# Optimization experiments

Measured on AMD Instinct MI355X. Metric: run time of the kernel, lower is better.

## Reference

```python
import jax, jax.numpy as jnp
import numpy as np

B = 256      # batch
C = 512      # num_classes (independent heads)
F = 768      # BERT pooler_output dim (hard-coded in module)
D = 512      # dense_layer_size


def setup_inputs() -> dict:
    key = jax.random.key(0)
    ks = jax.random.split(key, 7)
    s1 = 1.0 / np.sqrt(F)
    s2 = 1.0 / np.sqrt(D)
    return {
        "x":  jax.random.normal(ks[0], (B, F), dtype=jnp.float32),
        "W1": jax.random.normal(ks[1], (C, F, D), dtype=jnp.float32) * s1,
        "b1": jax.random.normal(ks[2], (C, D), dtype=jnp.float32) * s1,
        "W2": jax.random.normal(ks[3], (C, D, D), dtype=jnp.float32) * s2,
        "b2": jax.random.normal(ks[4], (C, D), dtype=jnp.float32) * s2,
        "W3": jax.random.normal(ks[5], (C, D, 2), dtype=jnp.float32) * s2,
        "b3": jax.random.normal(ks[6], (C, 2), dtype=jnp.float32) * s2,
    }


def reference(x, W1, b1, W2, b2, W3, b3):
    # Batched version of the per-class Python loop:
    # each head: Linear(F,D)-ReLU-(Dropout=identity in eval)-Linear(D,D)-ReLU-Linear(D,2)
    h = jax.nn.relu(jnp.einsum('bf,cfd->bcd', x, W1) + b1[None])        # [B, C, D]
    h = jax.nn.relu(jnp.einsum('bcd,cde->bce', h, W2) + b2[None])        # [B, C, D]
    out = jnp.einsum('bcd,cde->bce', h, W3) + b3[None]                   # [B, C, 2]
    return out
```

## Files before the change

### kernel.cpp

```cpp
#include <hip/hip_runtime.h>
#include <stdint.h>

typedef float f32x4 __attribute__((ext_vector_type(4)));
typedef float f32x2 __attribute__((ext_vector_type(2)));
typedef short bf16x8 __attribute__((ext_vector_type(8)));
typedef uint32_t u32x4 __attribute__((ext_vector_type(4)));

__device__ __forceinline__ uint32_t bf16_rne(float f) {
  uint32_t x = __float_as_uint(f);
  return (x + 0x7FFFu + ((x >> 16) & 1u)) >> 16;
}

__device__ __forceinline__ void ldsbar() {
  asm volatile("s_waitcnt lgkmcnt(0)\n\ts_barrier" ::: "memory");
}

__global__ void cast_x_kernel(const float* __restrict__ x,
                              uint32_t* __restrict__ xb, int n2) {
  int i = blockIdx.x * 256 + threadIdx.x;
  if (i >= n2) return;
  f32x2 v = *(const f32x2*)(x + 2 * i);
  xb[i] = bf16_rne(v[0]) | (bf16_rne(v[1]) << 16);
}

template <int K, int MODE>
__global__ __launch_bounds__(512, 4) void gemm_fused(
    const uint16_t* __restrict__ Abase, long long aClassStride,
    const float* __restrict__ Wbase, const float* __restrict__ biasBase,
    uint16_t* __restrict__ Hout, const float* __restrict__ W3base,
    float* __restrict__ part) {
  constexpr int NT = K / 64;
  __shared__ uint8_t smem[16384];

  const int tid = threadIdx.x;
  const int bid = blockIdx.x;
  const int logical = ((bid & 7) << 9) | (bid >> 3);
  const int c = logical >> 3;
  const int nt = logical & 7;
  const int n0 = nt * 64;

  const uint16_t* Ab = Abase + (size_t)c * (size_t)aClassStride;
  const float* Wc = Wbase + (size_t)c * (K * 512) + n0;

  const int l = tid & 63, w = tid >> 6;
  const int lr = l & 15, lg = l >> 4;

  const uint16_t* Ap = Ab + (size_t)(w * 32 + lr) * K + lg * 8;

  f32x4 acc[2][4];
#pragma unroll
  for (int i = 0; i < 2; i++)
#pragma unroll
    for (int j = 0; j < 4; j++) acc[i][j] = {0.f, 0.f, 0.f, 0.f};

  auto loadB = [&](int ts, float* g) {
    const float* Ws = Wc + (size_t)(ts * 64 + w * 8) * 512 + l;
#pragma unroll
    for (int r = 0; r < 8; r++) g[r] = Ws[(size_t)r * 512];
  };
  auto loadA = [&](int ts, bf16x8* as) {
#pragma unroll
    for (int kk = 0; kk < 2; ++kk)
#pragma unroll
      for (int mf = 0; mf < 2; mf++)
        as[kk * 2 + mf] =
            *(const bf16x8*)(Ap + ts * 64 + kk * 32 + (size_t)mf * 16 * K);
  };
  auto writeB = [&](const float* g, int buf) {
    u32x4 p;
#pragma unroll
    for (int j = 0; j < 4; j++)
      p[j] = bf16_rne(g[2 * j]) | (bf16_rne(g[2 * j + 1]) << 16);
    *(u32x4*)(smem + buf * 8192 + l * 128 + ((w ^ (l & 7)) << 4)) = p;
  };
  auto comp = [&](int buf, const bf16x8* as) {
    const uint8_t* s = smem + buf * 8192;
#pragma unroll
    for (int kk = 0; kk < 2; ++kk) {
      const int kx = ((lg * 16) ^ ((lr & 7) << 4)) ^ (kk << 6);
      bf16x8 b[4];
#pragma unroll
      for (int nf = 0; nf < 4; nf++)
        b[nf] = *(const bf16x8*)(s + (nf * 16 + lr) * 128 + kx);
#pragma unroll
      for (int mf = 0; mf < 2; mf++)
#pragma unroll
        for (int nf = 0; nf < 4; nf++)
          acc[mf][nf] = __builtin_amdgcn_mfma_f32_16x16x32_bf16(
              as[kk * 2 + mf], b[nf], acc[mf][nf], 0, 0, 0);
    }
  };

  float g[3][8];
  bf16x8 a[2][4];
  loadB(0, g[0]);
  loadB(1, g[1]);
  loadA(0, a[0]);
  writeB(g[0], 0);
  loadA(1, a[1]);
  loadB(2, g[2]);
  ldsbar();

#pragma unroll
  for (int t = 0; t < NT; ++t) {
    comp(t & 1, a[t & 1]);
    if (t + 1 < NT) writeB(g[(t + 1) % 3], (t + 1) & 1);
    if (t + 2 < NT) loadA(t + 2, a[t & 1]);
    if (t + 3 < NT) loadB(t + 3, g[t % 3]);
    if (t + 1 < NT) ldsbar();
  }

  float bv[4];
#pragma unroll
  for (int nf = 0; nf < 4; nf++)
    bv[nf] = biasBase[c * 512 + n0 + nf * 16 + lr];

  if constexpr (MODE == 0) {
    uint16_t* Oc = Hout + (size_t)c * 131072 + n0;
#pragma unroll
    for (int mf = 0; mf < 2; mf++)
#pragma unroll
      for (int nf = 0; nf < 4; nf++)
#pragma unroll
        for (int r = 0; r < 4; r++) {
          int m = w * 32 + mf * 16 + lg * 4 + r;
          float v = fmaxf(acc[mf][nf][r] + bv[nf], 0.f);
          Oc[(size_t)m * 512 + nf * 16 + lr] = (uint16_t)bf16_rne(v);
        }
  } else {
    float w30[4], w31[4];
#pragma unroll
    for (int nf = 0; nf < 4; nf++) {
      f32x2 t = *(const f32x2*)(W3base +
                                ((size_t)c * 512 + n0 + nf * 16 + lr) * 2);
      w30[nf] = t[0];
      w31[nf] = t[1];
    }
#pragma unroll
    for (int mf = 0; mf < 2; mf++)
#pragma unroll
      for (int r = 0; r < 4; r++) {
        float s0 = 0.f, s1 = 0.f;
#pragma unroll
        for (int nf = 0; nf < 4; nf++) {
          float v = fmaxf(acc[mf][nf][r] + bv[nf], 0.f);
          s0 += v * w30[nf];
          s1 += v * w31[nf];
        }
#pragma unroll
        for (int d = 1; d < 16; d <<= 1) {
          s0 += __shfl_xor(s0, d);
          s1 += __shfl_xor(s1, d);
        }
        if (lr == 0) {
          int m = w * 32 + mf * 16 + lg * 4 + r;
          *(f32x2*)(part + (((size_t)c * 256 + m) * 8 + nt) * 2) =
              f32x2{s0, s1};
        }
      }
  }
}

__global__ __launch_bounds__(512) void reduce_out(
    const float* __restrict__ part, const float* __restrict__ b3,
    float* __restrict__ out) {
  const int b = blockIdx.x, c = threadIdx.x;
  const f32x4* p = (const f32x4*)(part + ((size_t)c * 256 + b) * 16);
  f32x4 v0 = p[0], v1 = p[1], v2 = p[2], v3 = p[3];
  float s0 = b3[c * 2] + v0[0] + v0[2] + v1[0] + v1[2] + v2[0] + v2[2] +
             v3[0] + v3[2];
  float s1 = b3[c * 2 + 1] + v0[1] + v0[3] + v1[1] + v1[3] + v2[1] + v2[3] +
             v3[1] + v3[3];
  *(f32x2*)(out + ((size_t)b * 512 + c) * 2) = f32x2{s0, s1};
}

extern "C" void kernel_launch(void* const* d_in, const int* in_sizes, int n_in,
                              void* d_out, int out_size, void* d_ws,
                              size_t ws_size, hipStream_t stream) {
  const float* x = (const float*)d_in[0];
  const float* W1 = (const float*)d_in[1];
  const float* b1 = (const float*)d_in[2];
  const float* W2 = (const float*)d_in[3];
  const float* b2 = (const float*)d_in[4];
  const float* W3 = (const float*)d_in[5];
  const float* b3 = (const float*)d_in[6];
  float* out = (float*)d_out;

  uint8_t* ws = (uint8_t*)d_ws;
  const size_t xb_off = 0;
  const size_t h1_off = 393216;
  const size_t part_off = h1_off + 134217728;
  const size_t need = part_off + 8388608;
  if (ws_size < need) return;

  uint32_t* xb = (uint32_t*)(ws + xb_off);
  uint16_t* h1 = (uint16_t*)(ws + h1_off);
  float* part = (float*)(ws + part_off);

  cast_x_kernel<<<dim3(384), dim3(256), 0, stream>>>(x, xb, 98304);
  gemm_fused<768, 0><<<dim3(4096), dim3(512), 0, stream>>>(
      (const uint16_t*)xb, 0LL, W1, b1, h1, nullptr, nullptr);
  gemm_fused<512, 1><<<dim3(4096), dim3(512), 0, stream>>>(
      h1, 131072LL, W2, b2, nullptr, W3, part);
  reduce_out<<<dim3(256), dim3(512), 0, stream>>>(part, b3, out);
}
```

Measured before the change: 464.8 us.

## Store hidden activations in MFMA fragment order via LDS-staged transpose

The first GEMM now stages its bf16 outputs through a swizzled shared-memory tile and writes them out as 16-byte vectors in a fragment-ordered layout. The second GEMM can then read its A operands as contiguous per-lane vectors instead of strided row loads. B conversion uses the packed v_cvt_pk_bf16_f32 instruction instead of manual rounding, and prologue loads are reordered. Shared memory grows to 48KB and launch bounds drop to 2 blocks per SM, which may reduce occupancy.

```diff
diff --git a/kernel.cpp b/kernel.cpp
--- a/kernel.cpp
+++ b/kernel.cpp
@@ -24,13 +24,12 @@
 }
 
 template <int K, int MODE>
-__global__ __launch_bounds__(512, 4) void gemm_fused(
-    const uint16_t* __restrict__ Abase, long long aClassStride,
-    const float* __restrict__ Wbase, const float* __restrict__ biasBase,
-    uint16_t* __restrict__ Hout, const float* __restrict__ W3base,
-    float* __restrict__ part) {
+__global__ __launch_bounds__(512, 2) void gemm_fused(
+    const uint16_t* __restrict__ Abase, const float* __restrict__ Wbase,
+    const float* __restrict__ biasBase, uint16_t* __restrict__ Hout,
+    const float* __restrict__ W3base, float* __restrict__ part) {
   constexpr int NT = K / 64;
-  __shared__ uint8_t smem[16384];
+  __shared__ uint8_t smem[49152];
 
   const int tid = threadIdx.x;
   const int bid = blockIdx.x;
@@ -39,13 +38,15 @@
   const int nt = logical & 7;
   const int n0 = nt * 64;
 
-  const uint16_t* Ab = Abase + (size_t)c * (size_t)aClassStride;
   const float* Wc = Wbase + (size_t)c * (K * 512) + n0;
-
   const int l = tid & 63, w = tid >> 6;
   const int lr = l & 15, lg = l >> 4;
 
-  const uint16_t* Ap = Ab + (size_t)(w * 32 + lr) * K + lg * 8;
+  const uint16_t* Ap;
+  if constexpr (MODE == 0)
+    Ap = Abase + (size_t)(w * 32 + lr) * 768 + lg * 8;
+  else
+    Ap = Abase + (size_t)c * 131072 + w * 1024 + l * 8;
 
   f32x4 acc[2][4];
 #pragma unroll
@@ -54,23 +55,30 @@
     for (int j = 0; j < 4; j++) acc[i][j] = {0.f, 0.f, 0.f, 0.f};
 
   auto loadB = [&](int ts, float* g) {
-    const float* Ws = Wc + (size_t)(ts * 64 + w * 8) * 512 + l;
-#pragma unroll
-    for (int r = 0; r < 8; r++) g[r] = Ws[(size_t)r * 512];
+    const float* p = Wc + (size_t)(ts * 64 + w * 8) * 512 + l;
+#pragma unroll
+    for (int r = 0; r < 8; r++) g[r] = p[(size_t)r * 512];
   };
   auto loadA = [&](int ts, bf16x8* as) {
 #pragma unroll
     for (int kk = 0; kk < 2; ++kk)
 #pragma unroll
-      for (int mf = 0; mf < 2; mf++)
-        as[kk * 2 + mf] =
-            *(const bf16x8*)(Ap + ts * 64 + kk * 32 + (size_t)mf * 16 * K);
+      for (int mf = 0; mf < 2; mf++) {
+        if constexpr (MODE == 0)
+          as[kk * 2 + mf] = *(const bf16x8*)(Ap + ts * 64 + kk * 32 +
+                                             (size_t)mf * 16 * 768);
+        else
+          as[kk * 2 + mf] =
+              *(const bf16x8*)(Ap + ts * 16384 + kk * 8192 + mf * 512);
+      }
   };
   auto writeB = [&](const float* g, int buf) {
-    u32x4 p;
-#pragma unroll
-    for (int j = 0; j < 4; j++)
-      p[j] = bf16_rne(g[2 * j]) | (bf16_rne(g[2 * j + 1]) << 16);
+    uint32_t p0, p1, p2, p3;
+    asm("v_cvt_pk_bf16_f32 %0, %1, %2" : "=v"(p0) : "v"(g[0]), "v"(g[1]));
+    asm("v_cvt_pk_bf16_f32 %0, %1, %2" : "=v"(p1) : "v"(g[2]), "v"(g[3]));
+    asm("v_cvt_pk_bf16_f32 %0, %1, %2" : "=v"(p2) : "v"(g[4]), "v"(g[5]));
+    asm("v_cvt_pk_bf16_f32 %0, %1, %2" : "=v"(p3) : "v"(g[6]), "v"(g[7]));
+    u32x4 p = {p0, p1, p2, p3};
     *(u32x4*)(smem + buf * 8192 + l * 128 + ((w ^ (l & 7)) << 4)) = p;
   };
   auto comp = [&](int buf, const bf16x8* as) {
@@ -96,9 +104,9 @@
   loadB(0, g[0]);
   loadB(1, g[1]);
   loadA(0, a[0]);
+  loadB(2, g[2]);
+  loadA(1, a[1]);
   writeB(g[0], 0);
-  loadA(1, a[1]);
-  loadB(2, g[2]);
   ldsbar();
 
 #pragma unroll
@@ -116,17 +124,28 @@
     bv[nf] = biasBase[c * 512 + n0 + nf * 16 + lr];
 
   if constexpr (MODE == 0) {
-    uint16_t* Oc = Hout + (size_t)c * 131072 + n0;
+    uint8_t* T = smem + 16384 + w * 4096;
 #pragma unroll
     for (int mf = 0; mf < 2; mf++)
 #pragma unroll
       for (int nf = 0; nf < 4; nf++)
 #pragma unroll
         for (int r = 0; r < 4; r++) {
-          int m = w * 32 + mf * 16 + lg * 4 + r;
+          int m = mf * 16 + lg * 4 + r;
           float v = fmaxf(acc[mf][nf][r] + bv[nf], 0.f);
-          Oc[(size_t)m * 512 + nf * 16 + lr] = (uint16_t)bf16_rne(v);
-        }
+          *(uint16_t*)(T + m * 128 + (((nf * 16 + lr) * 2) ^ ((m & 7) << 4))) =
+              (uint16_t)bf16_rne(v);
+        }
+    uint16_t* Hc = Hout + (size_t)c * 131072 + nt * 16384 + w * 1024 + l * 8;
+#pragma unroll
+    for (int kk = 0; kk < 2; kk++)
+#pragma unroll
+      for (int mf = 0; mf < 2; mf++) {
+        int m = mf * 16 + lr;
+        bf16x8 hv = *(const bf16x8*)(T + m * 128 +
+                                     ((kk * 64 + lg * 16) ^ ((m & 7) << 4)));
+        *(bf16x8*)(Hc + kk * 8192 + mf * 512) = hv;
+      }
   } else {
     float w30[4], w31[4];
 #pragma unroll
@@ -194,13 +213,13 @@
   if (ws_size < need) return;
 
   uint32_t* xb = (uint32_t*)(ws + xb_off);
-  uint16_t* h1 = (uint16_t*)(ws + h1_off);
+  uint16_t* h1f = (uint16_t*)(ws + h1_off);
   float* part = (float*)(ws + part_off);
 
   cast_x_kernel<<<dim3(384), dim3(256), 0, stream>>>(x, xb, 98304);
   gemm_fused<768, 0><<<dim3(4096), dim3(512), 0, stream>>>(
-      (const uint16_t*)xb, 0LL, W1, b1, h1, nullptr, nullptr);
+      (const uint16_t*)xb, W1, b1, h1f, nullptr, nullptr);
   gemm_fused<512, 1><<<dim3(4096), dim3(512), 0, stream>>>(
-      h1, 131072LL, W2, b2, nullptr, W3, part);
+      h1f, W2, b2, nullptr, W3, part);
   reduce_out<<<dim3(256), dim3(512), 0, stream>>>(part, b3, out);
 }
```

Measured after the change: 423.0 us. 9.0% less time.
